# Kernel tuning notes

Measured on AMD Instinct MI355X. Metric: run time of the kernel, lower is better.

Reference implementation:

```python
import jax, jax.numpy as jnp
import numpy as np

B, L, C = 8, 8192, 384


def setup_inputs() -> dict:
    key = jax.random.key(0)
    mem = jax.random.normal(key, (B, L, C), dtype=jnp.float32)
    return {"mem": mem}


def _channel_offsets(num_units: int) -> np.ndarray:
    # Replicates baseFilter construction: groups of 3 channels get
    # [0,1,0] (identity), [1,0,0] (read t-1), [0,0,1] (read t+1);
    # leftover channels (num_units % 3) get identity.
    full = (num_units // 3) * 3
    off = np.zeros(num_units, dtype=np.int32)
    off[1:full:3] = -1  # kernel [1,0,0]: out[t] = in[t-1]
    off[2:full:3] = 1   # kernel [0,0,1]: out[t] = in[t+1]
    return off


def reference(mem):
    b, l, c = mem.shape
    off = _channel_offsets(c)  # static per-channel shift offsets
    # SAME padding of the 1x3 depthwise conv == zero-pad 1 on each side of L
    padded = jnp.pad(mem, ((0, 0), (1, 1), (0, 0)))  # [B, L+2, C]
    # gather index t+1+off[c] into the padded sequence
    idx = np.arange(l)[:, None] + 1 + off[None, :]  # [L, C], static
    idx = jnp.asarray(idx)[None, :, :]  # [1, L, C]
    return jnp.take_along_axis(padded, idx, axis=1)  # [B, L, C]
```

## Files before the change

### kernel.cpp

```cpp
#include <hip/hip_runtime.h>


constexpr int kB = 8;
constexpr int kL = 8192;
constexpr int kC = 384;
constexpr int kV = 4;
constexpr int kCV = kC / kV;
constexpr int kTotalV = kB * kL * kCV;

typedef __attribute__((ext_vector_type(4))) float f32x4;

__global__ __launch_bounds__(256) void ShiftLayer_66932770341347_kernel(
    const f32x4* __restrict__ in, f32x4* __restrict__ out) {
  int idx = blockIdx.x * 256 + threadIdx.x;
  if (idx >= kTotalV) return;

  int v = idx % kCV;
  int t = (idx / kCV) % kL;

  const f32x4 zero = {0.f, 0.f, 0.f, 0.f};
  f32x4 cur = in[idx];
  f32x4 prev = (t > 0)      ? in[idx - kCV] : zero;
  f32x4 next = (t < kL - 1) ? in[idx + kCV] : zero;

  int m0 = v % 3;

  f32x4 o;
#pragma unroll
  for (int i = 0; i < kV; ++i) {
    int m = m0 + i;
    m = (m >= 3) ? m - 3 : m;
    m = (m >= 3) ? m - 3 : m;
    o[i] = (m == 0) ? cur[i] : ((m == 1) ? prev[i] : next[i]);
  }
  out[idx] = o;
}

extern "C" void kernel_launch(void* const* d_in, const int* in_sizes, int n_in,
                              void* d_out, int out_size, void* d_ws, size_t ws_size,
                              hipStream_t stream) {
  const f32x4* in = reinterpret_cast<const f32x4*>(d_in[0]);
  f32x4* out = reinterpret_cast<f32x4*>(d_out);

  constexpr int kThreads = 256;
  constexpr int kBlocks = (kTotalV + kThreads - 1) / kThreads;
  ShiftLayer_66932770341347_kernel<<<kBlocks, kThreads, 0, stream>>>(in, out);
}
```

Baseline: 169.5 us.

## Process eight timesteps per thread with sliding register window and nontemporal stores

Each thread now walks eight consecutive timesteps for one channel vector and keeps prev/cur/next in registers, so each input row is loaded about once instead of three times. Output writes use nontemporal stores to avoid polluting cache. This cuts redundant load instructions and thread count, but reduces parallelism eightfold and gives each thread strided accesses across time, which may lower memory-level parallelism. The kernel is bandwidth bound (~200MB traffic), and the redundant loads mostly hit cache already.

```diff
diff --git a/kernel.cpp b/kernel.cpp
--- a/kernel.cpp
+++ b/kernel.cpp
@@ -6,34 +6,51 @@
 constexpr int kC = 384;
 constexpr int kV = 4;
 constexpr int kCV = kC / kV;
-constexpr int kTotalV = kB * kL * kCV;
+constexpr int kT = 8;
+constexpr int kTB = kL / kT;
+constexpr int kThreads = 256;
+constexpr int kTotalThreads = kB * kTB * kCV;
+constexpr int kBlocks = kTotalThreads / kThreads;
 
 typedef __attribute__((ext_vector_type(4))) float f32x4;
 
 __global__ __launch_bounds__(256) void ShiftLayer_66932770341347_kernel(
     const f32x4* __restrict__ in, f32x4* __restrict__ out) {
-  int idx = blockIdx.x * 256 + threadIdx.x;
-  if (idx >= kTotalV) return;
+  int idx = blockIdx.x * kThreads + threadIdx.x;
 
   int v = idx % kCV;
-  int t = (idx / kCV) % kL;
+  int rest = idx / kCV;
+  int tb = rest % kTB;
+  int b = rest / kTB;
+  int t0 = tb * kT;
+
+  const f32x4* __restrict__ base = in + (long)b * (kL * kCV) + v;
+  f32x4* __restrict__ obase = out + (long)b * (kL * kCV) + v;
 
   const f32x4 zero = {0.f, 0.f, 0.f, 0.f};
-  f32x4 cur = in[idx];
-  f32x4 prev = (t > 0)      ? in[idx - kCV] : zero;
-  f32x4 next = (t < kL - 1) ? in[idx + kCV] : zero;
 
   int m0 = v % 3;
 
-  f32x4 o;
+  f32x4 prev = (t0 > 0) ? base[(long)(t0 - 1) * kCV] : zero;
+  f32x4 cur = base[(long)t0 * kCV];
+
 #pragma unroll
-  for (int i = 0; i < kV; ++i) {
-    int m = m0 + i;
-    m = (m >= 3) ? m - 3 : m;
-    m = (m >= 3) ? m - 3 : m;
-    o[i] = (m == 0) ? cur[i] : ((m == 1) ? prev[i] : next[i]);
+  for (int i = 0; i < kT; ++i) {
+    int t = t0 + i;
+    f32x4 next = (t + 1 < kL) ? base[(long)(t + 1) * kCV] : zero;
+
+    f32x4 o;
+#pragma unroll
+    for (int j = 0; j < kV; ++j) {
+      int m = m0 + j;
+      m = (m >= 3) ? m - 3 : m;
+      o[j] = (m == 0) ? cur[j] : ((m == 1) ? prev[j] : next[j]);
+    }
+    __builtin_nontemporal_store(o, &obase[(long)t * kCV]);
+
+    prev = cur;
+    cur = next;
   }
-  out[idx] = o;
 }
 
 extern "C" void kernel_launch(void* const* d_in, const int* in_sizes, int n_in,
@@ -41,8 +58,5 @@
                               hipStream_t stream) {
   const f32x4* in = reinterpret_cast<const f32x4*>(d_in[0]);
   f32x4* out = reinterpret_cast<f32x4*>(d_out);
-
-  constexpr int kThreads = 256;
-  constexpr int kBlocks = (kTotalV + kThreads - 1) / kThreads;
   ShiftLayer_66932770341347_kernel<<<kBlocks, kThreads, 0, stream>>>(in, out);
 }
```

New measurement: 180.6 us. 6.6% more time.

## Stage time-row tiles with halo in LDS to avoid triple global reads

Applied to the files above, without the earlier changes.

Each block now loads 8 time rows plus one halo row on each side into shared memory, then builds each output from the LDS neighbours instead of issuing three global loads per vector. This is meant to cut redundant global and L2 traffic, since each input is otherwise read three times. In exchange it adds a block barrier, 25% halo overfetch and an LDS round trip to a kernel that is purely bandwidth-bound, where cache already absorbs much of the reuse.

```diff
diff --git a/kernel.cpp b/kernel.cpp
--- a/kernel.cpp
+++ b/kernel.cpp
@@ -6,34 +6,60 @@
 constexpr int kC = 384;
 constexpr int kV = 4;
 constexpr int kCV = kC / kV;
-constexpr int kTotalV = kB * kL * kCV;
+constexpr int kTB = 8;
+constexpr int kRows = kTB + 2;
+constexpr int kStage = kRows * kCV;
+constexpr int kThreads = 256;
+constexpr int kBlocks = kB * (kL / kTB);
 
 typedef __attribute__((ext_vector_type(4))) float f32x4;
 
 __global__ __launch_bounds__(256) void ShiftLayer_66932770341347_kernel(
     const f32x4* __restrict__ in, f32x4* __restrict__ out) {
-  int idx = blockIdx.x * 256 + threadIdx.x;
-  if (idx >= kTotalV) return;
+  __shared__ f32x4 lds[kStage];
 
-  int v = idx % kCV;
-  int t = (idx / kCV) % kL;
+  int tb = blockIdx.x % (kL / kTB);
+  int b = blockIdx.x / (kL / kTB);
+  long rowbase = (long)(tb * kTB) * kCV;
+
+  const f32x4* __restrict__ base = in + (long)b * (kL * kCV);
+  f32x4* __restrict__ obase = out + (long)b * (kL * kCV) + rowbase;
 
   const f32x4 zero = {0.f, 0.f, 0.f, 0.f};
-  f32x4 cur = in[idx];
-  f32x4 prev = (t > 0)      ? in[idx - kCV] : zero;
-  f32x4 next = (t < kL - 1) ? in[idx + kCV] : zero;
 
-  int m0 = v % 3;
+#pragma unroll
+  for (int k = 0; k < 4; ++k) {
+    int s = threadIdx.x + k * kThreads;
+    if (s < kStage) {
+      long g = rowbase - kCV + s;
+      f32x4 val = zero;
+      if (g >= 0 && g < (long)kL * kCV) val = base[g];
+      lds[s] = val;
+    }
+  }
+  __syncthreads();
 
-  f32x4 o;
+  int m0 = threadIdx.x % 3;
 #pragma unroll
-  for (int i = 0; i < kV; ++i) {
-    int m = m0 + i;
-    m = (m >= 3) ? m - 3 : m;
-    m = (m >= 3) ? m - 3 : m;
-    o[i] = (m == 0) ? cur[i] : ((m == 1) ? prev[i] : next[i]);
+  for (int k = 0; k < 3; ++k) {
+    int j = threadIdx.x + k * kThreads;
+    f32x4 prev = lds[j];
+    f32x4 cur = lds[j + kCV];
+    f32x4 next = lds[j + 2 * kCV];
+
+    int mb = m0 + k;
+    mb = (mb >= 3) ? mb - 3 : mb;
+
+    f32x4 o;
+#pragma unroll
+    for (int i = 0; i < kV; ++i) {
+      int m = mb + i;
+      m = (m >= 3) ? m - 3 : m;
+      m = (m >= 3) ? m - 3 : m;
+      o[i] = (m == 0) ? cur[i] : ((m == 1) ? prev[i] : next[i]);
+    }
+    obase[j] = o;
   }
-  out[idx] = o;
 }
 
 extern "C" void kernel_launch(void* const* d_in, const int* in_sizes, int n_in,
@@ -41,8 +67,5 @@
                               hipStream_t stream) {
   const f32x4* in = reinterpret_cast<const f32x4*>(d_in[0]);
   f32x4* out = reinterpret_cast<f32x4*>(d_out);
-
-  constexpr int kThreads = 256;
-  constexpr int kBlocks = (kTotalV + kThreads - 1) / kThreads;
   ShiftLayer_66932770341347_kernel<<<kBlocks, kThreads, 0, stream>>>(in, out);
 }
```

Result: slower. 178.1 us (+5.1%).

## Use persistent grid-stride loop with double-buffered register prefetch

Applied to the files above, without the earlier changes.

Replaces the one-thread-per-vector launch with a fixed grid of 2048 blocks. Each thread loops over 12 strided elements and prefetches the next iteration's prev/cur/next loads into a second register set while the current output is computed. Index arithmetic is updated incrementally rather than with per-element divisions, and boundary loads are clamped so they never read out of range. The aim is more memory-level parallelism per thread and lower launch and index overhead, at the cost of higher register use and less scheduling freedom for the hardware.

```diff
diff --git a/kernel.cpp b/kernel.cpp
--- a/kernel.cpp
+++ b/kernel.cpp
@@ -6,34 +6,76 @@
 constexpr int kC = 384;
 constexpr int kV = 4;
 constexpr int kCV = kC / kV;
+constexpr int kThreads = 256;
+constexpr int kBlocks = 2048;
 constexpr int kTotalV = kB * kL * kCV;
+constexpr int kStride = kBlocks * kThreads;
+constexpr int kIter = kTotalV / kStride;
+constexpr int kQStep = kStride / kCV;
+constexpr int kVStep = kStride % kCV;
 
 typedef __attribute__((ext_vector_type(4))) float f32x4;
 
 __global__ __launch_bounds__(256) void ShiftLayer_66932770341347_kernel(
     const f32x4* __restrict__ in, f32x4* __restrict__ out) {
-  int idx = blockIdx.x * 256 + threadIdx.x;
-  if (idx >= kTotalV) return;
+  const f32x4 zero = {0.f, 0.f, 0.f, 0.f};
 
-  int v = idx % kCV;
-  int t = (idx / kCV) % kL;
+  int idx = blockIdx.x * kThreads + threadIdx.x;
 
-  const f32x4 zero = {0.f, 0.f, 0.f, 0.f};
-  f32x4 cur = in[idx];
-  f32x4 prev = (t > 0)      ? in[idx - kCV] : zero;
-  f32x4 next = (t < kL - 1) ? in[idx + kCV] : zero;
-
+  int q = idx / kCV;
+  int v = idx - q * kCV;
+  int t = q & (kL - 1);
   int m0 = v % 3;
 
-  f32x4 o;
+  f32x4 rp[2], rc[2], rn[2];
+  int tS[2], oS[2], mS[2];
+
+  {
+    int pi = (t == 0) ? idx : idx - kCV;
+    int ni = (t == kL - 1) ? idx : idx + kCV;
+    rp[0] = in[pi];
+    rc[0] = in[idx];
+    rn[0] = in[ni];
+    tS[0] = t; oS[0] = idx; mS[0] = m0;
+  }
+
 #pragma unroll
-  for (int i = 0; i < kV; ++i) {
-    int m = m0 + i;
-    m = (m >= 3) ? m - 3 : m;
-    m = (m >= 3) ? m - 3 : m;
-    o[i] = (m == 0) ? cur[i] : ((m == 1) ? prev[i] : next[i]);
+  for (int k = 0; k < kIter; ++k) {
+    const int cur = k & 1, nxt = cur ^ 1;
+
+    if (k + 1 < kIter) {
+      idx += kStride;
+      v += kVStep;
+      int carry = (v >= kCV) ? 1 : 0;
+      v -= carry ? kCV : 0;
+      q += kQStep + carry;
+      t = q & (kL - 1);
+      m0 += 2;
+      m0 = (m0 >= 3) ? m0 - 3 : m0;
+
+      int pi = (t == 0) ? idx : idx - kCV;
+      int ni = (t == kL - 1) ? idx : idx + kCV;
+      rp[nxt] = in[pi];
+      rc[nxt] = in[idx];
+      rn[nxt] = in[ni];
+      tS[nxt] = t; oS[nxt] = idx; mS[nxt] = m0;
+    }
+
+    f32x4 P = (tS[cur] == 0) ? zero : rp[cur];
+    f32x4 C = rc[cur];
+    f32x4 N = (tS[cur] == kL - 1) ? zero : rn[cur];
+
+    int mb = mS[cur];
+    f32x4 o;
+#pragma unroll
+    for (int j = 0; j < kV; ++j) {
+      int m = mb + j;
+      m = (m >= 3) ? m - 3 : m;
+      m = (m >= 3) ? m - 3 : m;
+      o[j] = (m == 0) ? C[j] : ((m == 1) ? P[j] : N[j]);
+    }
+    out[oS[cur]] = o;
   }
-  out[idx] = o;
 }
 
 extern "C" void kernel_launch(void* const* d_in, const int* in_sizes, int n_in,
@@ -41,8 +83,5 @@
                               hipStream_t stream) {
   const f32x4* in = reinterpret_cast<const f32x4*>(d_in[0]);
   f32x4* out = reinterpret_cast<f32x4*>(d_out);
-
-  constexpr int kThreads = 256;
-  constexpr int kBlocks = (kTotalV + kThreads - 1) / kThreads;
   ShiftLayer_66932770341347_kernel<<<kBlocks, kThreads, 0, stream>>>(in, out);
 }
```

Measured after the change: 174.7 us. 1.03x slower.
